# Kernel optimization log

Hardware: AMD Instinct MI355X
Metric: run time of the kernel (lower is better)

## Reference

```python
import jax, jax.numpy as jnp
import numpy as np

L, D, H, DFF = 4, 1024, 16, 4096
DH = D // H
B, T = 2, 2048
EPS = 1e-5


def setup_inputs() -> dict:
    key = jax.random.key(0)
    ks = jax.random.split(key, 16)
    xav_a = (6.0 / (D + D)) ** 0.5      # xavier_uniform for square DxD
    xav_f1 = (6.0 / (D + DFF)) ** 0.5
    xav_f2 = (6.0 / (DFF + D)) ** 0.5
    def u(k, shape, a):
        return jax.random.uniform(k, shape, jnp.float32, -a, a)
    inp = {
        "x": jax.random.normal(ks[0], (B, T, D), jnp.float32),
        "mask": jnp.ones((B, T), jnp.int32),
        # attention projections, torch Linear layout [out, in]
        "Wq": u(ks[1], (L, D, D), xav_a), "bq": jnp.zeros((L, D), jnp.float32),
        "Wk": u(ks[2], (L, D, D), xav_a), "bk": jnp.zeros((L, D), jnp.float32),
        "Wv": u(ks[3], (L, D, D), xav_a), "bv": jnp.zeros((L, D), jnp.float32),
        "Wo": u(ks[4], (L, D, D), xav_a), "bo": jnp.zeros((L, D), jnp.float32),
        # FFN
        "fc1_w": u(ks[5], (L, DFF, D), xav_f1), "fc1_b": jnp.zeros((L, DFF), jnp.float32),
        "fc2_w": u(ks[6], (L, D, DFF), xav_f2), "fc2_b": jnp.zeros((L, D), jnp.float32),
        # LayerNorms
        "ln1_g": jnp.ones((L, D), jnp.float32), "ln1_b": jnp.zeros((L, D), jnp.float32),
        "ln2_g": jnp.ones((L, D), jnp.float32), "ln2_b": jnp.zeros((L, D), jnp.float32),
        "lnf_g": jnp.ones((D,), jnp.float32), "lnf_b": jnp.zeros((D,), jnp.float32),
    }
    return inp


def _layernorm(x, g, b):
    mu = jnp.mean(x, axis=-1, keepdims=True)
    var = jnp.mean(jnp.square(x - mu), axis=-1, keepdims=True)
    return (x - mu) * jax.lax.rsqrt(var + EPS) * g + b


def _encoder_forward(x, mask, Wq, bq, Wk, bk, Wv, bv, Wo, bo,
                     fc1_w, fc1_b, fc2_w, fc2_b,
                     ln1_g, ln1_b, ln2_g, ln2_b, lnf_g, lnf_b):
    keep = mask.astype(bool)[:, None, None, :]  # [B,1,1,Tk]
    scale = 1.0 / (DH ** 0.5)
    for l in range(L):
        # --- multi-head self-attention ---
        q = (jnp.einsum('btd,ed->bte', x, Wq[l]) + bq[l]).reshape(B, T, H, DH).transpose(0, 2, 1, 3)
        k = (jnp.einsum('btd,ed->bte', x, Wk[l]) + bk[l]).reshape(B, T, H, DH).transpose(0, 2, 1, 3)
        v = (jnp.einsum('btd,ed->bte', x, Wv[l]) + bv[l]).reshape(B, T, H, DH).transpose(0, 2, 1, 3)
        logits = jnp.einsum('bhqd,bhkd->bhqk', q, k) * scale
        logits = jnp.where(keep, logits, -jnp.inf)
        attn = jax.nn.softmax(logits, axis=-1)
        ctx = jnp.einsum('bhqk,bhkd->bhqd', attn, v).transpose(0, 2, 1, 3).reshape(B, T, D)
        attn_out = jnp.einsum('btd,ed->bte', ctx, Wo[l]) + bo[l]
        x = _layernorm(x + attn_out, ln1_g[l], ln1_b[l])
        # --- feed-forward (exact GELU, like torch nn.GELU default) ---
        h = jax.nn.gelu(jnp.einsum('btd,fd->btf', x, fc1_w[l]) + fc1_b[l], approximate=False)
        ff_out = jnp.einsum('btf,df->btd', h, fc2_w[l]) + fc2_b[l]
        x = _layernorm(x + ff_out, ln2_g[l], ln2_b[l])
    return _layernorm(x, lnf_g, lnf_b)


def reference(x, mask, Wq, bq, Wk, bk, Wv, bv, Wo, bo,
              fc1_w, fc1_b, fc2_w, fc2_b,
              ln1_g, ln1_b, ln2_g, ln2_b, lnf_g, lnf_b):
    return _encoder_forward(x, mask, Wq, bq, Wk, bk, Wv, bv, Wo, bo,
                            fc1_w, fc1_b, fc2_w, fc2_b,
                            ln1_g, ln1_b, ln2_g, ln2_b, lnf_g, lnf_b)
```

## Files before the change

kernel.cpp:

```cpp
#include <hip/hip_runtime.h>
#include <hip/hip_bf16.h>
#include <cstdint>

#define BB 2
#define TT 2048
#define DD 1024
#define HH 16
#define DHH 64
#define DFF 4096
#define LL 4
#define MM (BB*TT)
#define NT (TT/64)

typedef __attribute__((ext_vector_type(8))) short short8v;
typedef __attribute__((ext_vector_type(4))) short short4v;
typedef __attribute__((ext_vector_type(4))) float floatx4;

typedef __attribute__((address_space(3))) void lds_void;
typedef const __attribute__((address_space(1))) void glb_void;

__device__ __forceinline__ void gload_lds16(const void* g, void* l) {
  __builtin_amdgcn_global_load_lds((glb_void*)g, (lds_void*)l, 16, 0, 0);
}

__device__ __forceinline__ float bf2f(short s) {
  union { unsigned u; float f; } v; v.u = ((unsigned)(unsigned short)s) << 16; return v.f;
}
__device__ __forceinline__ short f2bf(float f) {
  union { float f; unsigned u; } v; v.f = f;
  unsigned r = (v.u + 0x7fffu + ((v.u >> 16) & 1u)) >> 16;
  return (short)r;
}
__device__ __forceinline__ unsigned pack2bf(float a, float b) {
  __hip_bfloat162 h = __float22bfloat162_rn(make_float2(a, b));
  return *reinterpret_cast<unsigned*>(&h);
}
__device__ __forceinline__ float fexp2(float x) {
  float r; asm("v_exp_f32 %0, %1" : "=v"(r) : "v"(x)); return r;
}
__device__ __forceinline__ float max3f(float a, float b, float c) {
  float r; asm("v_max3_f32 %0, %1, %2, %3" : "=v"(r) : "v"(a), "v"(b), "v"(c)); return r;
}
__device__ __forceinline__ float gelu_fast(float x) {
  const float u = x * x;
  const float w = fmaf(u, -0.10294537f, -2.302203f);
  const float t = fexp2(w * x);
  return x * __builtin_amdgcn_rcpf(1.f + t);
}

#define SCL2 0.18033688011112042f
__device__ __forceinline__ short8v scale8(short8v v) {
  short8v r;
#pragma unroll
  for (int i = 0; i < 8; ++i) r[i] = f2bf(bf2f(v[i]) * SCL2);
  return r;
}

#define SEG (DD*DD)
#define WTOT (4*SEG + 2*DFF*DD)
__global__ __launch_bounds__(256) void cast_layer(
    const float* __restrict__ wq, const float* __restrict__ wk,
    const float* __restrict__ wv, const float* __restrict__ wo,
    const float* __restrict__ f1, const float* __restrict__ f2,
    short* __restrict__ dst)
{
  const int i = (blockIdx.x * 256 + threadIdx.x) * 4;
  const float* src; int off;
  if      (i <     SEG) { src = wq; off = i; }
  else if (i < 2 * SEG) { src = wk; off = i - SEG; }
  else if (i < 3 * SEG) { src = wv; off = i - 2 * SEG; }
  else if (i < 4 * SEG) { src = wo; off = i - 3 * SEG; }
  else if (i < 4 * SEG + DFF * DD) { src = f1; off = i - 4 * SEG; }
  else { src = f2; off = i - 4 * SEG - DFF * DD; }
  const float4 v = *(const float4*)(src + off);
  short4v o; o[0] = f2bf(v.x); o[1] = f2bf(v.y); o[2] = f2bf(v.z); o[3] = f2bf(v.w);
  *(short4v*)(dst + i) = o;
}

template<int GELU, int QKV>
__global__ __launch_bounds__(512, 2) void gemm256(
    const short* __restrict__ A, const short* __restrict__ W,
    const float* __restrict__ b0, const float* __restrict__ b1,
    const float* __restrict__ b2, short* __restrict__ C,
    int M, int N, int K)
{
  __shared__ __align__(16) short lds[65536];
  const int t = threadIdx.x;
  const int lane = t & 63, wave = t >> 6;
  const int wm = wave >> 2, wn = wave & 3;
  const int l15 = lane & 15, lg = lane >> 4;

  const int nwg = gridDim.x * gridDim.y;
  const int bid0 = blockIdx.y * gridDim.x + blockIdx.x;
  const int q8 = nwg >> 3;
  const int lid = (bid0 & 7) * q8 + (bid0 >> 3);
  const int bx = lid % gridDim.x, by = lid / gridDim.x;

  const size_t abase = (size_t)by * 256 * K;
  const size_t wbase = (size_t)bx * 256 * K;

  floatx4 acc[8][4];
  floatx4 zero = {0.f, 0.f, 0.f, 0.f};
#pragma unroll
  for (int m = 0; m < 8; ++m)
#pragma unroll
    for (int n = 0; n < 4; ++n) acc[m][n] = zero;

#define STG_A(sl_, h_, u_) do {                                                \
    _Pragma("unroll")                                                          \
    for (int j_ = 0; j_ < 2; ++j_) {                                           \
      const int c_ = j_ * 512 + t, r_ = c_ >> 3;                               \
      const int kc_ = (c_ & 7) ^ (r_ & 7);                                     \
      gload_lds16(A + abase + (size_t)((h_) * 128 + r_) * K + (u_) * 64 + kc_ * 8, \
                  &lds[(sl_) * 16384 + (h_) * 8192 + (j_ * 512 + wave * 64) * 8]); \
    } } while (0)
#define STG_B(sl_, h_, u_) do {                                                \
    _Pragma("unroll")                                                          \
    for (int j_ = 0; j_ < 2; ++j_) {                                           \
      const int c_ = j_ * 512 + t, r_ = c_ >> 3;                               \
      const int kc_ = (c_ & 7) ^ (r_ & 7);                                     \
      gload_lds16(W + wbase + (size_t)((h_) * 128 + r_) * K + (u_) * 64 + kc_ * 8, \
                  &lds[32768 + (sl_) * 16384 + (h_) * 8192 + (j_ * 512 + wave * 64) * 8]); \
    } } while (0)

  const int NTK = K >> 6;
  STG_A(0, 0, 0); STG_A(0, 1, 0); STG_B(0, 0, 0); STG_B(0, 1, 0);

  for (int u = 0; u < NTK; ++u) {
    const int sl = u & 1, ns = sl ^ 1;
    const int aoff = sl * 16384 + wm * 8192;
    const int boff = 32768 + sl * 16384 + (wn >> 1) * 8192;
    short8v bfr[4][2];
#pragma unroll
    for (int p = 0; p < 4; ++p) {
      if (p == 0) {
        if (u + 1 < NTK) {
          STG_A(ns, 0, u + 1);
          asm volatile("s_waitcnt vmcnt(2)" ::: "memory");
        } else {
          asm volatile("s_waitcnt vmcnt(0)" ::: "memory");
        }
        __builtin_amdgcn_s_barrier();
#pragma unroll
        for (int n = 0; n < 4; ++n)
#pragma unroll
          for (int kk = 0; kk < 2; ++kk) {
            const int rl = (wn & 1) * 64 + n * 16 + l15;
            bfr[n][kk] = *(const short8v*)&lds[boff + rl * 64 + ((kk * 4 + lg) ^ (rl & 7)) * 8];
          }
      } else if (p == 1) { if (u + 1 < NTK) STG_A(ns, 1, u + 1); }
      else if (p == 2)   { if (u + 1 < NTK) STG_B(ns, 0, u + 1); }
      else               { if (u + 1 < NTK) STG_B(ns, 1, u + 1); }

      short8v af[2][2];
#pragma unroll
      for (int i = 0; i < 2; ++i)
#pragma unroll
        for (int kk = 0; kk < 2; ++kk) {
          const int rl = (2 * p + i) * 16 + l15;
          af[i][kk] = *(const short8v*)&lds[aoff + rl * 64 + ((kk * 4 + lg) ^ (rl & 7)) * 8];
        }
      asm volatile("s_waitcnt lgkmcnt(0)" ::: "memory");
      __builtin_amdgcn_s_setprio(1);
#pragma unroll
      for (int kk = 0; kk < 2; ++kk)
#pragma unroll
        for (int i = 0; i < 2; ++i)
#pragma unroll
          for (int n = 0; n < 4; ++n)
            acc[2 * p + i][n] = __builtin_amdgcn_mfma_f32_16x16x32_bf16(
                af[i][kk], bfr[n][kk], acc[2 * p + i][n], 0, 0, 0);
      __builtin_amdgcn_s_setprio(0);
      __builtin_amdgcn_s_barrier();
    }
  }
#undef STG_A
#undef STG_B

  const float* bp;
  int cbase = bx * 256 + wn * 64;
  if (QKV) {
    const int seg = cbase >> 10;
    bp = (seg == 0) ? b0 : (seg == 1 ? b1 : b2);
    cbase -= seg << 10;
  } else {
    bp = b0;
  }
  float bv[4];
#pragma unroll
  for (int n = 0; n < 4; ++n)
    bv[n] = bp[cbase + n * 16 + l15];
#pragma unroll
  for (int m = 0; m < 8; ++m)
#pragma unroll
    for (int jj = 0; jj < 4; ++jj) {
      const int row = by * 256 + wm * 128 + m * 16 + lg * 4 + jj;
      short* cp = C + (size_t)row * N + bx * 256 + wn * 64 + l15;
#pragma unroll
      for (int n = 0; n < 4; ++n) {
        float v = acc[m][n][jj] + bv[n];
        if (GELU) v = gelu_fast(v);
        cp[n * 16] = f2bf(v);
      }
    }
}

template<int GELU>
__global__ __launch_bounds__(512, 2) void gemm128(
    const short* __restrict__ A, const short* __restrict__ W,
    const float* __restrict__ bias, short* __restrict__ C,
    int M, int N, int K)
{
  __shared__ __align__(16) short lds[49152];
  const int t = threadIdx.x;
  const int lane = t & 63, wave = t >> 6;
  const int wm = wave >> 2, wn = wave & 3;
  const int l15 = lane & 15, lg = lane >> 4;

  const int nwg = gridDim.x * gridDim.y;
  const int bid0 = blockIdx.y * gridDim.x + blockIdx.x;
  const int q8 = nwg >> 3;
  const int lid = (bid0 & 7) * q8 + (bid0 >> 3);
  const int bx = lid % gridDim.x, by = lid / gridDim.x;

  const size_t abase = (size_t)by * 128 * K;
  const size_t wbase = (size_t)bx * 128 * K;

  floatx4 acc[4][2];
  floatx4 zero = {0.f, 0.f, 0.f, 0.f};
#pragma unroll
  for (int m = 0; m < 4; ++m)
#pragma unroll
    for (int n = 0; n < 2; ++n) acc[m][n] = zero;

#define STG128(sl_, u_) do {                                                   \
    _Pragma("unroll")                                                          \
    for (int j_ = 0; j_ < 2; ++j_) {                                           \
      const int c_ = j_ * 512 + t, r_ = c_ >> 3;                               \
      const int kc_ = (c_ & 7) ^ (r_ & 7);                                     \
      gload_lds16(A + abase + (size_t)r_ * K + (u_) * 64 + kc_ * 8,            \
                  &lds[(sl_) * 8192 + (j_ * 512 + wave * 64) * 8]);            \
      gload_lds16(W + wbase + (size_t)r_ * K + (u_) * 64 + kc_ * 8,            \
                  &lds[24576 + (sl_) * 8192 + (j_ * 512 + wave * 64) * 8]);    \
    } } while (0)

  const int NTK = K >> 6;
  STG128(0, 0);
  STG128(1, 1);

  for (int u = 0; u < NTK; ++u) {
    const int sl = u % 3;
    if (u + 1 < NTK) asm volatile("s_waitcnt vmcnt(4)" ::: "memory");
    else             asm volatile("s_waitcnt vmcnt(0)" ::: "memory");
    __builtin_amdgcn_s_barrier();
    if (u + 2 < NTK) STG128((u + 2) % 3, u + 2);

    short8v bfr[2][2], af[4][2];
#pragma unroll
    for (int n = 0; n < 2; ++n)
#pragma unroll
      for (int kk = 0; kk < 2; ++kk) {
        const int rl = wn * 32 + n * 16 + l15;
        bfr[n][kk] = *(const short8v*)&lds[24576 + sl * 8192 + rl * 64 + ((kk * 4 + lg) ^ (rl & 7)) * 8];
      }
#pragma unroll
    for (int m = 0; m < 4; ++m)
#pragma unroll
      for (int kk = 0; kk < 2; ++kk) {
        const int rl = wm * 32 + ((m & 1) * 16) + l15 + (m >> 1) * 64;
        af[m][kk] = *(const short8v*)&lds[sl * 8192 + rl * 64 + ((kk * 4 + lg) ^ (rl & 7)) * 8];
      }
    asm volatile("s_waitcnt lgkmcnt(0)" ::: "memory");
    __builtin_amdgcn_s_setprio(1);
#pragma unroll
    for (int kk = 0; kk < 2; ++kk)
#pragma unroll
      for (int m = 0; m < 4; ++m)
#pragma unroll
        for (int n = 0; n < 2; ++n)
          acc[m][n] = __builtin_amdgcn_mfma_f32_16x16x32_bf16(af[m][kk], bfr[n][kk], acc[m][n], 0, 0, 0);
    __builtin_amdgcn_s_setprio(0);
  }
#undef STG128

  float bv[2];
#pragma unroll
  for (int n = 0; n < 2; ++n)
    bv[n] = bias[bx * 128 + wn * 32 + n * 16 + l15];
#pragma unroll
  for (int m = 0; m < 4; ++m)
#pragma unroll
    for (int jj = 0; jj < 4; ++jj) {
      const int row = by * 128 + wm * 32 + (m & 1) * 16 + (m >> 1) * 64 + lg * 4 + jj;
      short* cp = C + (size_t)row * N + bx * 128 + wn * 32 + l15;
#pragma unroll
      for (int n = 0; n < 2; ++n) {
        float v = acc[m][n][jj] + bv[n];
        if (GELU) v = gelu_fast(v);
        cp[n * 16] = f2bf(v);
      }
    }
}

__global__ __launch_bounds__(256) void transpose_v(
    const short* __restrict__ qkv, short* __restrict__ vt)
{
  __shared__ short tile[64][65];
  const int tb = blockIdx.x, h = blockIdx.y, b = blockIdx.z;
  const int t = threadIdx.x;
  const int r = t >> 2, c4 = (t & 3) * 16;
  const short* src = qkv + ((size_t)(b * TT + tb * 64 + r)) * 3072 + 2048 + h * 64 + c4;
#pragma unroll
  for (int i = 0; i < 16; ++i) tile[r][c4 + i] = src[i];
  __syncthreads();
  short* dst = vt + ((size_t)((b * HH + h) * 64 + r)) * TT + tb * 64 + c4;
#pragma unroll
  for (int i = 0; i < 16; ++i) dst[i] = tile[c4 + i][r];
}

#define PSTR 72
__global__ __launch_bounds__(512, 4) void flash_attn(
    const short* __restrict__ qkv, const short* __restrict__ vt,
    const int* __restrict__ mask, short* __restrict__ ctx)
{
  const int t = threadIdx.x;
  const int lane = t & 63, wave = t >> 6;
  const int l15 = lane & 15, lg = lane >> 4;

  const int bid0 = blockIdx.x + gridDim.x * (blockIdx.y + gridDim.y * blockIdx.z);
  const int lid = (bid0 & 7) * 64 + (bid0 >> 3);
  const int qb = lid & 15, h = (lid >> 4) & 15, b = lid >> 8;

  __shared__ __align__(16) short Ks[2][64 * 64];
  __shared__ __align__(16) short Vs[2][64 * 64];
  __shared__ __align__(16) short p_lds[8][16 * PSTR];
  short* prow = p_lds[wave];

  const short* qp = qkv + ((size_t)(b * TT + qb * 128 + wave * 16 + l15)) * 3072 + h * 64;
  const short8v qf0 = scale8(*(const short8v*)(qp + lg * 8));
  const short8v qf1 = scale8(*(const short8v*)(qp + 32 + lg * 8));

  const short* kbase = qkv + (size_t)b * TT * 3072 + 1024 + h * 64;
  const short* vtb   = vt + ((size_t)(b * HH + h)) * 64 * TT;

  const int srow = lane >> 3;
  const int scol = (lane & 7) ^ (srow & 7);

  float m_run = -3e30f, l_run = 0.f;
  floatx4 zero = {0.f, 0.f, 0.f, 0.f};
  floatx4 o[4];
#pragma unroll
  for (int n = 0; n < 4; ++n) o[n] = zero;

#define STAGE_KV(bufi, kb_) do {                                             \
    const int r_ = wave * 8 + srow;                                          \
    gload_lds16(kbase + (size_t)((kb_) * 64 + r_) * 3072 + scol * 8,         \
                &Ks[bufi][wave * 512]);                                      \
    gload_lds16(vtb + (size_t)r_ * TT + (kb_) * 64 + scol * 8,               \
                &Vs[bufi][wave * 512]);                                      \
  } while (0)

  STAGE_KV(0, 0);
  int buf = 0;
  for (int kb = 0; kb < NT; ++kb) {
    if (kb + 1 < NT) {
      STAGE_KV(buf ^ 1, kb + 1);
      asm volatile("s_waitcnt vmcnt(2)" ::: "memory");
    } else {
      asm volatile("s_waitcnt vmcnt(0)" ::: "memory");
    }
    __builtin_amdgcn_s_barrier();

    float cm[4][4];
#pragma unroll
    for (int n = 0; n < 4; ++n) {
      const int4 mv = *(const int4*)&mask[b * TT + kb * 64 + n * 16 + lg * 4];
      cm[n][0] = mv.x ? 0.f : -1.5e30f; cm[n][1] = mv.y ? 0.f : -1.5e30f;
      cm[n][2] = mv.z ? 0.f : -1.5e30f; cm[n][3] = mv.w ? 0.f : -1.5e30f;
    }

    floatx4 s[4];
#pragma unroll
    for (int n = 0; n < 4; ++n) {
      const int row = n * 16 + l15;
      const int ch0 = lg ^ (row & 7);
      const int ch1 = (lg + 4) ^ (row & 7);
      const short8v kf0 = *(const short8v*)&Ks[buf][row * 64 + ch0 * 8];
      const short8v kf1 = *(const short8v*)&Ks[buf][row * 64 + ch1 * 8];
      floatx4 a = zero;
      a = __builtin_amdgcn_mfma_f32_16x16x32_bf16(kf0, qf0, a, 0, 0, 0);
      a = __builtin_amdgcn_mfma_f32_16x16x32_bf16(kf1, qf1, a, 0, 0, 0);
      s[n] = a;
    }
#pragma unroll
    for (int n = 0; n < 4; ++n)
#pragma unroll
      for (int jj = 0; jj < 4; ++jj) s[n][jj] += cm[n][jj];

    const float t0 = max3f(s[0][0], s[0][1], s[0][2]);
    const float t1 = max3f(s[0][3], s[1][0], s[1][1]);
    const float t2 = max3f(s[1][2], s[1][3], s[2][0]);
    const float t3 = max3f(s[2][1], s[2][2], s[2][3]);
    const float t4 = max3f(s[3][0], s[3][1], s[3][2]);
    float mx = fmaxf(max3f(t0, t1, t2), max3f(t3, t4, s[3][3]));
    mx = fmaxf(mx, __shfl_xor(mx, 16, 64));
    mx = fmaxf(mx, __shfl_xor(mx, 32, 64));

    const bool defer = __all(mx - m_run <= 11.5f);
    const float mnew = defer ? m_run : fmaxf(m_run, mx);
    float ps[4];
#pragma unroll
    for (int n = 0; n < 4; ++n) {
      s[n][0] = fexp2(s[n][0] - mnew);
      s[n][1] = fexp2(s[n][1] - mnew);
      s[n][2] = fexp2(s[n][2] - mnew);
      s[n][3] = fexp2(s[n][3] - mnew);
      ps[n] = (s[n][0] + s[n][1]) + (s[n][2] + s[n][3]);
    }
    float sum = (ps[0] + ps[1]) + (ps[2] + ps[3]);
    sum += __shfl_xor(sum, 16, 64);
    sum += __shfl_xor(sum, 32, 64);
    if (defer) {
      l_run += sum;
    } else {
      const float al = fexp2(m_run - mnew);
      l_run = l_run * al + sum;
      m_run = mnew;
      float alo[4];
#pragma unroll
      for (int jj = 0; jj < 4; ++jj) alo[jj] = __shfl(al, lg * 4 + jj, 16);
#pragma unroll
      for (int n = 0; n < 4; ++n)
#pragma unroll
        for (int jj = 0; jj < 4; ++jj) o[n][jj] *= alo[jj];
    }

#pragma unroll
    for (int n = 0; n < 4; ++n) {
      const unsigned u0 = pack2bf(s[n][0], s[n][1]);
      const unsigned u1 = pack2bf(s[n][2], s[n][3]);
      *(uint2*)&prow[l15 * PSTR + n * 16 + lg * 4] = make_uint2(u0, u1);
    }
    const short8v pf0 = *(const short8v*)&prow[l15 * PSTR + lg * 8];
    const short8v pf1 = *(const short8v*)&prow[l15 * PSTR + 32 + lg * 8];

#pragma unroll
    for (int n = 0; n < 4; ++n) {
      const int row = n * 16 + l15;
      const int ch0 = lg ^ (row & 7);
      const int ch1 = (lg + 4) ^ (row & 7);
      const short8v vf0 = *(const short8v*)&Vs[buf][row * 64 + ch0 * 8];
      const short8v vf1 = *(const short8v*)&Vs[buf][row * 64 + ch1 * 8];
      o[n] = __builtin_amdgcn_mfma_f32_16x16x32_bf16(pf0, vf0, o[n], 0, 0, 0);
      o[n] = __builtin_amdgcn_mfma_f32_16x16x32_bf16(pf1, vf1, o[n], 0, 0, 0);
    }
    asm volatile("" ::: "memory");
    __builtin_amdgcn_s_barrier();
    buf ^= 1;
  }
#undef STAGE_KV

#pragma unroll
  for (int jj = 0; jj < 4; ++jj) {
    const float inv = 1.f / __shfl(l_run, lg * 4 + jj, 16);
    const int row = qb * 128 + wave * 16 + lg * 4 + jj;
#pragma unroll
    for (int n = 0; n < 4; ++n)
      ctx[((size_t)(b * TT + row)) * DD + h * 64 + n * 16 + l15] = f2bf(o[n][jj] * inv);
  }
}

__global__ __launch_bounds__(256) void add_ln(
    const float* __restrict__ xres, const short* __restrict__ add,
    const float* __restrict__ g, const float* __restrict__ bb,
    float* __restrict__ outf, short* __restrict__ outb)
{
  const int row = blockIdx.x, t = threadIdx.x;
  const int lane = t & 63, wave = t >> 6;
  const float4 xv = *(const float4*)(xres + (size_t)row * DD + t * 4);
  float y[4] = { xv.x, xv.y, xv.z, xv.w };
  if (add) {
    const short4v av = *(const short4v*)(add + (size_t)row * DD + t * 4);
#pragma unroll
    for (int i = 0; i < 4; ++i) y[i] += bf2f(av[i]);
  }
  float s = y[0] + y[1] + y[2] + y[3];
  float ss = y[0]*y[0] + y[1]*y[1] + y[2]*y[2] + y[3]*y[3];
#pragma unroll
  for (int off = 32; off >= 1; off >>= 1) {
    s  += __shfl_xor(s, off, 64);
    ss += __shfl_xor(ss, off, 64);
  }
  __shared__ float red[2][4];
  if (lane == 0) { red[0][wave] = s; red[1][wave] = ss; }
  __syncthreads();
  s  = red[0][0] + red[0][1] + red[0][2] + red[0][3];
  ss = red[1][0] + red[1][1] + red[1][2] + red[1][3];
  const float mu = s * (1.f / DD);
  const float var = ss * (1.f / DD) - mu * mu;
  const float rs = rsqrtf(var + 1e-5f);
  const float4 gv = *(const float4*)(g + t * 4);
  const float4 bv = *(const float4*)(bb + t * 4);
  float o[4];
  o[0] = (y[0] - mu) * rs * gv.x + bv.x;
  o[1] = (y[1] - mu) * rs * gv.y + bv.y;
  o[2] = (y[2] - mu) * rs * gv.z + bv.z;
  o[3] = (y[3] - mu) * rs * gv.w + bv.w;
  if (outf) *(float4*)(outf + (size_t)row * DD + t * 4) = make_float4(o[0], o[1], o[2], o[3]);
  if (outb) {
    short4v ov;
#pragma unroll
    for (int i = 0; i < 4; ++i) ov[i] = f2bf(o[i]);
    *(short4v*)(outb + (size_t)row * DD + t * 4) = ov;
  }
}

__global__ __launch_bounds__(256) void cast_in(
    const float* __restrict__ x, float* __restrict__ xf,
    short* __restrict__ xb)
{
  const int i = (blockIdx.x * 256 + threadIdx.x) * 4;
  const float4 v = *(const float4*)(x + i);
  *(float4*)(xf + i) = v;
  short4v o; o[0] = f2bf(v.x); o[1] = f2bf(v.y); o[2] = f2bf(v.z); o[3] = f2bf(v.w);
  *(short4v*)(xb + i) = o;
}

extern "C" void kernel_launch(void* const* d_in, const int* in_sizes, int n_in,
                              void* d_out, int out_size, void* d_ws, size_t ws_size,
                              hipStream_t stream) {
  const float* x   = (const float*)d_in[0];
  const int* mask  = (const int*)d_in[1];
  const float* Wq  = (const float*)d_in[2];
  const float* bq  = (const float*)d_in[3];
  const float* Wk  = (const float*)d_in[4];
  const float* bk  = (const float*)d_in[5];
  const float* Wv  = (const float*)d_in[6];
  const float* bv  = (const float*)d_in[7];
  const float* Wo  = (const float*)d_in[8];
  const float* bo  = (const float*)d_in[9];
  const float* f1w = (const float*)d_in[10];
  const float* f1b = (const float*)d_in[11];
  const float* f2w = (const float*)d_in[12];
  const float* f2b = (const float*)d_in[13];
  const float* l1g = (const float*)d_in[14];
  const float* l1b = (const float*)d_in[15];
  const float* l2g = (const float*)d_in[16];
  const float* l2b = (const float*)d_in[17];
  const float* lfg = (const float*)d_in[18];
  const float* lfb = (const float*)d_in[19];
  float* out = (float*)d_out;

  char* ws = (char*)d_ws;
  const size_t MB = 1u << 20;
  float* xf   = (float*)(ws);
  short* xb   = (short*)(ws + 16 * MB);
  short* qkv  = (short*)(ws + 24 * MB);
  short* vt_  = (short*)(ws + 48 * MB);
  short* ctx  = (short*)(ws + 56 * MB);
  short* tmp  = (short*)(ws + 64 * MB);
  short* wbuf = (short*)(ws + 72 * MB);
  short* hb   = qkv;

  cast_in<<<(MM * DD) / (256 * 4), 256, 0, stream>>>(x, xf, xb);

  for (int l = 0; l < LL; ++l) {
    cast_layer<<<WTOT / (256 * 4), 256, 0, stream>>>(
        Wq + (size_t)l * SEG, Wk + (size_t)l * SEG, Wv + (size_t)l * SEG, Wo + (size_t)l * SEG,
        f1w + (size_t)l * DFF * DD, f2w + (size_t)l * DD * DFF, wbuf);
    const short* wqkv_b = wbuf;
    const short* wo_b   = wbuf + 3 * SEG;
    const short* f1_b   = wbuf + 4 * SEG;
    const short* f2_b   = wbuf + 4 * SEG + DFF * DD;

    gemm256<0,1><<<dim3(3072 / 256, MM / 256), 512, 0, stream>>>(
        xb, wqkv_b, bq + l * DD, bk + l * DD, bv + l * DD, qkv, MM, 3072, DD);
    transpose_v<<<dim3(TT / 64, HH, BB), 256, 0, stream>>>(qkv, vt_);
    flash_attn<<<dim3(TT / 128, HH, BB), 512, 0, stream>>>(qkv, vt_, mask, ctx);
    gemm128<0><<<dim3(DD / 128, MM / 128), 512, 0, stream>>>(ctx, wo_b, bo + l * DD, tmp, MM, DD, DD);
    add_ln<<<MM, 256, 0, stream>>>(xf, tmp, l1g + l * DD, l1b + l * DD, xf, xb);
    gemm256<1,0><<<dim3(DFF / 256, MM / 256), 512, 0, stream>>>(
        xb, f1_b, f1b + l * DFF, nullptr, nullptr, hb, MM, DFF, DD);
    gemm128<0><<<dim3(DD / 128, MM / 128), 512, 0, stream>>>(hb, f2_b, f2b + l * DD, tmp, MM, DD, DFF);
    add_ln<<<MM, 256, 0, stream>>>(xf, tmp, l2g + l * DD, l2b + l * DD, xf, xb);
  }
  add_ln<<<MM, 256, 0, stream>>>(xf, nullptr, lfg, lfb, out, nullptr);
}
```

Before: 942.2 us.

## Split-K the N=1024 projection GEMMs and fuse partial reduction into add+LayerNorm

```diff
diff --git a/kernel.cpp b/kernel.cpp
--- a/kernel.cpp
+++ b/kernel.cpp
@@ -205,11 +205,10 @@
     }
 }
 
-template<int GELU>
-__global__ __launch_bounds__(512, 2) void gemm128(
+__global__ __launch_bounds__(512, 2) void gemm128sk(
     const short* __restrict__ A, const short* __restrict__ W,
-    const float* __restrict__ bias, short* __restrict__ C,
-    int M, int N, int K)
+    short* __restrict__ P0, short* __restrict__ P1,
+    int M, int N, int K, int KH)
 {
   __shared__ __align__(16) short lds[49152];
   const int t = threadIdx.x;
@@ -217,14 +216,18 @@
   const int wm = wave >> 2, wn = wave & 3;
   const int l15 = lane & 15, lg = lane >> 4;
 
-  const int nwg = gridDim.x * gridDim.y;
-  const int bid0 = blockIdx.y * gridDim.x + blockIdx.x;
+  const int gx = gridDim.x, gy = gridDim.y;
+  const int nwg = gx * gy * gridDim.z;
+  const int bid0 = (blockIdx.z * gy + blockIdx.y) * gx + blockIdx.x;
   const int q8 = nwg >> 3;
   const int lid = (bid0 & 7) * q8 + (bid0 >> 3);
-  const int bx = lid % gridDim.x, by = lid / gridDim.x;
-
-  const size_t abase = (size_t)by * 128 * K;
-  const size_t wbase = (size_t)bx * 128 * K;
+  const int bx = lid % gx;
+  const int by = (lid / gx) % gy;
+  const int kz = lid / (gx * gy);
+  short* __restrict__ P = kz ? P1 : P0;
+
+  const size_t abase = (size_t)by * 128 * K + (size_t)kz * KH;
+  const size_t wbase = (size_t)bx * 128 * K + (size_t)kz * KH;
 
   floatx4 acc[4][2];
   floatx4 zero = {0.f, 0.f, 0.f, 0.f};
@@ -244,7 +247,7 @@
                   &lds[24576 + (sl_) * 8192 + (j_ * 512 + wave * 64) * 8]);    \
     } } while (0)
 
-  const int NTK = K >> 6;
+  const int NTK = KH >> 6;
   STG128(0, 0);
   STG128(1, 1);
 
@@ -283,22 +286,15 @@
   }
 #undef STG128
 
-  float bv[2];
-#pragma unroll
-  for (int n = 0; n < 2; ++n)
-    bv[n] = bias[bx * 128 + wn * 32 + n * 16 + l15];
 #pragma unroll
   for (int m = 0; m < 4; ++m)
 #pragma unroll
     for (int jj = 0; jj < 4; ++jj) {
       const int row = by * 128 + wm * 32 + (m & 1) * 16 + (m >> 1) * 64 + lg * 4 + jj;
-      short* cp = C + (size_t)row * N + bx * 128 + wn * 32 + l15;
-#pragma unroll
-      for (int n = 0; n < 2; ++n) {
-        float v = acc[m][n][jj] + bv[n];
-        if (GELU) v = gelu_fast(v);
-        cp[n * 16] = f2bf(v);
-      }
+      short* cp = P + (size_t)row * N + bx * 128 + wn * 32 + l15;
+#pragma unroll
+      for (int n = 0; n < 2; ++n)
+        cp[n * 16] = f2bf(acc[m][n][jj]);
     }
 }
 
@@ -468,6 +464,52 @@
     for (int n = 0; n < 4; ++n)
       ctx[((size_t)(b * TT + row)) * DD + h * 64 + n * 16 + l15] = f2bf(o[n][jj] * inv);
   }
+}
+
+__global__ __launch_bounds__(256) void add_ln2(
+    const float* __restrict__ xres, const short* __restrict__ p0,
+    const short* __restrict__ p1, const float* __restrict__ bvec,
+    const float* __restrict__ g, const float* __restrict__ bb,
+    float* __restrict__ outf, short* __restrict__ outb)
+{
+  const int row = blockIdx.x, t = threadIdx.x;
+  const int lane = t & 63, wave = t >> 6;
+  const float4 xv = *(const float4*)(xres + (size_t)row * DD + t * 4);
+  const short4v a0 = *(const short4v*)(p0 + (size_t)row * DD + t * 4);
+  const short4v a1 = *(const short4v*)(p1 + (size_t)row * DD + t * 4);
+  const float4 bvl = *(const float4*)(bvec + t * 4);
+  float y[4];
+  y[0] = xv.x + bf2f(a0[0]) + bf2f(a1[0]) + bvl.x;
+  y[1] = xv.y + bf2f(a0[1]) + bf2f(a1[1]) + bvl.y;
+  y[2] = xv.z + bf2f(a0[2]) + bf2f(a1[2]) + bvl.z;
+  y[3] = xv.w + bf2f(a0[3]) + bf2f(a1[3]) + bvl.w;
+  float s = y[0] + y[1] + y[2] + y[3];
+  float ss = y[0]*y[0] + y[1]*y[1] + y[2]*y[2] + y[3]*y[3];
+#pragma unroll
+  for (int off = 32; off >= 1; off >>= 1) {
+    s  += __shfl_xor(s, off, 64);
+    ss += __shfl_xor(ss, off, 64);
+  }
+  __shared__ float red[2][4];
+  if (lane == 0) { red[0][wave] = s; red[1][wave] = ss; }
+  __syncthreads();
+  s  = red[0][0] + red[0][1] + red[0][2] + red[0][3];
+  ss = red[1][0] + red[1][1] + red[1][2] + red[1][3];
+  const float mu = s * (1.f / DD);
+  const float var = ss * (1.f / DD) - mu * mu;
+  const float rs = rsqrtf(var + 1e-5f);
+  const float4 gv = *(const float4*)(g + t * 4);
+  const float4 bv = *(const float4*)(bb + t * 4);
+  float o[4];
+  o[0] = (y[0] - mu) * rs * gv.x + bv.x;
+  o[1] = (y[1] - mu) * rs * gv.y + bv.y;
+  o[2] = (y[2] - mu) * rs * gv.z + bv.z;
+  o[3] = (y[3] - mu) * rs * gv.w + bv.w;
+  *(float4*)(outf + (size_t)row * DD + t * 4) = make_float4(o[0], o[1], o[2], o[3]);
+  short4v ov;
+#pragma unroll
+  for (int i = 0; i < 4; ++i) ov[i] = f2bf(o[i]);
+  *(short4v*)(outb + (size_t)row * DD + t * 4) = ov;
 }
 
 __global__ __launch_bounds__(256) void add_ln(
@@ -558,7 +600,9 @@
   short* qkv  = (short*)(ws + 24 * MB);
   short* vt_  = (short*)(ws + 48 * MB);
   short* ctx  = (short*)(ws + 56 * MB);
-  short* tmp  = (short*)(ws + 64 * MB);
+  short* p0   = (short*)(ws + 64 * MB);
+  short* p1w  = qkv;
+  short* p1f  = ctx;
   short* wbuf = (short*)(ws + 72 * MB);
   short* hb   = qkv;
 
@@ -577,12 +621,12 @@
         xb, wqkv_b, bq + l * DD, bk + l * DD, bv + l * DD, qkv, MM, 3072, DD);
     transpose_v<<<dim3(TT / 64, HH, BB), 256, 0, stream>>>(qkv, vt_);
     flash_attn<<<dim3(TT / 128, HH, BB), 512, 0, stream>>>(qkv, vt_, mask, ctx);
-    gemm128<0><<<dim3(DD / 128, MM / 128), 512, 0, stream>>>(ctx, wo_b, bo + l * DD, tmp, MM, DD, DD);
-    add_ln<<<MM, 256, 0, stream>>>(xf, tmp, l1g + l * DD, l1b + l * DD, xf, xb);
+    gemm128sk<<<dim3(DD / 128, MM / 128, 2), 512, 0, stream>>>(ctx, wo_b, p0, p1w, MM, DD, DD, 512);
+    add_ln2<<<MM, 256, 0, stream>>>(xf, p0, p1w, bo + l * DD, l1g + l * DD, l1b + l * DD, xf, xb);
     gemm256<1,0><<<dim3(DFF / 256, MM / 256), 512, 0, stream>>>(
         xb, f1_b, f1b + l * DFF, nullptr, nullptr, hb, MM, DFF, DD);
-    gemm128<0><<<dim3(DD / 128, MM / 128), 512, 0, stream>>>(hb, f2_b, f2b + l * DD, tmp, MM, DD, DFF);
-    add_ln<<<MM, 256, 0, stream>>>(xf, tmp, l2g + l * DD, l2b + l * DD, xf, xb);
+    gemm128sk<<<dim3(DD / 128, MM / 128, 2), 512, 0, stream>>>(hb, f2_b, p0, p1f, MM, DD, DFF, 2048);
+    add_ln2<<<MM, 256, 0, stream>>>(xf, p0, p1f, f2b + l * DD, l2g + l * DD, l2b + l * DD, xf, xb);
   }
   add_ln<<<MM, 256, 0, stream>>>(xf, nullptr, lfg, lfb, out, nullptr);
 }
```

After: 972.0 us. 3.2% more time.

## Split flash attention over two KV halves and merge with combine kernel

Applied to the files above, without the earlier changes.

```diff
diff --git a/kernel.cpp b/kernel.cpp
--- a/kernel.cpp
+++ b/kernel.cpp
@@ -319,17 +319,19 @@
 }
 
 #define PSTR 72
-__global__ __launch_bounds__(512, 4) void flash_attn(
+__global__ __launch_bounds__(512, 3) void flash_attn(
     const short* __restrict__ qkv, const short* __restrict__ vt,
-    const int* __restrict__ mask, short* __restrict__ ctx)
+    const int* __restrict__ mask, short* __restrict__ pc, float2* __restrict__ ml)
 {
   const int t = threadIdx.x;
   const int lane = t & 63, wave = t >> 6;
   const int l15 = lane & 15, lg = lane >> 4;
 
   const int bid0 = blockIdx.x + gridDim.x * (blockIdx.y + gridDim.y * blockIdx.z);
-  const int lid = (bid0 & 7) * 64 + (bid0 >> 3);
-  const int qb = lid & 15, h = (lid >> 4) & 15, b = lid >> 8;
+  const int lid = (bid0 & 7) * 128 + (bid0 >> 3);
+  const int qb = lid & 15, h = (lid >> 4) & 15;
+  const int z = lid >> 8, b = z >> 1, half = z & 1;
+  const int kb0 = half * (NT / 2), kb1 = kb0 + NT / 2;
 
   __shared__ __align__(16) short Ks[2][64 * 64];
   __shared__ __align__(16) short Vs[2][64 * 64];
@@ -360,10 +362,10 @@
                 &Vs[bufi][wave * 512]);                                      \
   } while (0)
 
-  STAGE_KV(0, 0);
+  STAGE_KV(0, kb0);
   int buf = 0;
-  for (int kb = 0; kb < NT; ++kb) {
-    if (kb + 1 < NT) {
+  for (int kb = kb0; kb < kb1; ++kb) {
+    if (kb + 1 < kb1) {
       STAGE_KV(buf ^ 1, kb + 1);
       asm volatile("s_waitcnt vmcnt(2)" ::: "memory");
     } else {
@@ -460,14 +462,41 @@
   }
 #undef STAGE_KV
 
+  short* pch = pc + (size_t)half * MM * DD;
 #pragma unroll
   for (int jj = 0; jj < 4; ++jj) {
-    const float inv = 1.f / __shfl(l_run, lg * 4 + jj, 16);
+    const float inv = __builtin_amdgcn_rcpf(fmaxf(__shfl(l_run, lg * 4 + jj, 16), 1e-30f));
     const int row = qb * 128 + wave * 16 + lg * 4 + jj;
 #pragma unroll
     for (int n = 0; n < 4; ++n)
-      ctx[((size_t)(b * TT + row)) * DD + h * 64 + n * 16 + l15] = f2bf(o[n][jj] * inv);
-  }
+      pch[((size_t)(b * TT + row)) * DD + h * 64 + n * 16 + l15] = f2bf(o[n][jj] * inv);
+  }
+  if (lane < 16)
+    ml[((size_t)(half * BB + b) * HH + h) * TT + qb * 128 + wave * 16 + lane] =
+        make_float2(m_run, l_run);
+}
+
+__global__ __launch_bounds__(256) void combine_kv(
+    const short* __restrict__ pc, const float2* __restrict__ ml,
+    short* __restrict__ ctxc)
+{
+  const int row = blockIdx.x, t = threadIdx.x;
+  const int b = row >> 11, trow = row & (TT - 1);
+  const int h = t >> 4;
+  const float2 m0 = ml[((size_t)(0 * BB + b) * HH + h) * TT + trow];
+  const float2 m1 = ml[((size_t)(1 * BB + b) * HH + h) * TT + trow];
+  const float m = fmaxf(m0.x, m1.x);
+  const float w0 = fexp2(m0.x - m) * m0.y;
+  const float w1 = fexp2(m1.x - m) * m1.y;
+  const float d = __builtin_amdgcn_rcpf(w0 + w1);
+  const float a0 = w0 * d, a1 = w1 * d;
+  const short4v o0 = *(const short4v*)(pc + (size_t)row * DD + t * 4);
+  const short4v o1 = *(const short4v*)(pc + (size_t)MM * DD + (size_t)row * DD + t * 4);
+  short4v ov;
+#pragma unroll
+  for (int i = 0; i < 4; ++i)
+    ov[i] = f2bf(bf2f(o0[i]) * a0 + bf2f(o1[i]) * a1);
+  *(short4v*)(ctxc + (size_t)row * DD + t * 4) = ov;
 }
 
 __global__ __launch_bounds__(256) void add_ln(
@@ -516,12 +545,10 @@
 }
 
 __global__ __launch_bounds__(256) void cast_in(
-    const float* __restrict__ x, float* __restrict__ xf,
-    short* __restrict__ xb)
+    const float* __restrict__ x, short* __restrict__ xb)
 {
   const int i = (blockIdx.x * 256 + threadIdx.x) * 4;
   const float4 v = *(const float4*)(x + i);
-  *(float4*)(xf + i) = v;
   short4v o; o[0] = f2bf(v.x); o[1] = f2bf(v.y); o[2] = f2bf(v.z); o[3] = f2bf(v.w);
   *(short4v*)(xb + i) = o;
 }
@@ -557,12 +584,14 @@
   short* xb   = (short*)(ws + 16 * MB);
   short* qkv  = (short*)(ws + 24 * MB);
   short* vt_  = (short*)(ws + 48 * MB);
-  short* ctx  = (short*)(ws + 56 * MB);
-  short* tmp  = (short*)(ws + 64 * MB);
-  short* wbuf = (short*)(ws + 72 * MB);
+  short* pc   = (short*)(ws + 56 * MB);
+  float2* ml  = (float2*)(ws + 72 * MB);
+  short* wbuf = (short*)(ws + 73 * MB);
+  short* ctxc = qkv;
+  short* tmp  = pc;
   short* hb   = qkv;
 
-  cast_in<<<(MM * DD) / (256 * 4), 256, 0, stream>>>(x, xf, xb);
+  cast_in<<<(MM * DD) / (256 * 4), 256, 0, stream>>>(x, xb);
 
   for (int l = 0; l < LL; ++l) {
     cast_layer<<<WTOT / (256 * 4), 256, 0, stream>>>(
@@ -576,9 +605,10 @@
     gemm256<0,1><<<dim3(3072 / 256, MM / 256), 512, 0, stream>>>(
         xb, wqkv_b, bq + l * DD, bk + l * DD, bv + l * DD, qkv, MM, 3072, DD);
     transpose_v<<<dim3(TT / 64, HH, BB), 256, 0, stream>>>(qkv, vt_);
-    flash_attn<<<dim3(TT / 128, HH, BB), 512, 0, stream>>>(qkv, vt_, mask, ctx);
-    gemm128<0><<<dim3(DD / 128, MM / 128), 512, 0, stream>>>(ctx, wo_b, bo + l * DD, tmp, MM, DD, DD);
-    add_ln<<<MM, 256, 0, stream>>>(xf, tmp, l1g + l * DD, l1b + l * DD, xf, xb);
+    flash_attn<<<dim3(TT / 128, HH, BB * 2), 512, 0, stream>>>(qkv, vt_, mask, pc, ml);
+    combine_kv<<<MM, 256, 0, stream>>>(pc, ml, ctxc);
+    gemm128<0><<<dim3(DD / 128, MM / 128), 512, 0, stream>>>(ctxc, wo_b, bo + l * DD, tmp, MM, DD, DD);
+    add_ln<<<MM, 256, 0, stream>>>(l == 0 ? x : xf, tmp, l1g + l * DD, l1b + l * DD, xf, xb);
     gemm256<1,0><<<dim3(DFF / 256, MM / 256), 512, 0, stream>>>(
         xb, f1_b, f1b + l * DFF, nullptr, nullptr, hb, MM, DFF, DD);
     gemm128<0><<<dim3(DD / 128, MM / 128), 512, 0, stream>>>(hb, f2_b, f2b + l * DD, tmp, MM, DD, DFF);
```

Result: slower. 978.9 us (+3.9%).
